# Optimization experiments

Hardware: AMD Instinct MI355X
Metric: run time of the kernel (lower is better)

Reference implementation:

```python
import jax, jax.numpy as jnp
import numpy as np
import math

N, E, IN, OUT, T, R = 50000, 500000, 128, 128, 8, 8
SQRT_DK = math.sqrt(OUT)


def setup_inputs() -> dict:
    key = jax.random.key(0)
    ks = jax.random.split(key, 12)
    return {
        "h": jax.random.normal(ks[0], (N, IN), jnp.float32),
        "adj": jax.random.randint(ks[1], (2, E), 0, N),
        "edge_type": jax.random.randint(ks[2], (E,), 0, R),
        "node_type": jax.random.randint(ks[3], (N,), 0, T),
        "src_type": jax.random.randint(ks[4], (E,), 0, T),
        "dst_type": jax.random.randint(ks[5], (E,), 0, T),
        # params (torch.rand -> uniform[0,1), torch.ones -> ones)
        "k_weights": jax.random.uniform(ks[6], (T, IN, OUT), jnp.float32),
        "q_weights": jax.random.uniform(ks[7], (T, IN, OUT), jnp.float32),
        "v_weights": jax.random.uniform(ks[8], (T, IN, OUT), jnp.float32),
        "a_weights": jax.random.uniform(ks[9], (T, OUT, OUT), jnp.float32),
        "relation_pri": jnp.ones((R, 1), jnp.float32),
        "relation_att": jax.random.uniform(ks[10], (R, OUT, OUT), jnp.float32),
        "relation_msg": jax.random.uniform(ks[11], (R, OUT, OUT), jnp.float32),
        "skip": jnp.ones((T,), jnp.float32),
    }


def _per_type(x, W, types):
    # x: [N,d], W: [T,d,f], types: [N] -> [N,f]
    # project by every type then select; avoids materializing a [N,d,f] gather
    all_proj = jnp.einsum('nd,tdf->tnf', x, W)  # [T,N,f]
    return all_proj[types, jnp.arange(x.shape[0])]


def _segment_softmax(scores, seg, num_segments):
    m = jax.ops.segment_max(scores, seg, num_segments=num_segments)
    m = jnp.where(jnp.isfinite(m), m, 0.0)  # empty segments
    ex = jnp.exp(scores - m[seg])
    denom = jax.ops.segment_sum(ex, seg, num_segments=num_segments)
    return ex / denom[seg]


def reference(h, adj, edge_type, node_type, src_type, dst_type,
              k_weights, q_weights, v_weights, a_weights,
              relation_pri, relation_att, relation_msg, skip):
    n = h.shape[0]
    src, dst = adj[0], adj[1]
    # per-node-type K/Q/V projections
    k = _per_type(h, k_weights, node_type)  # [N,OUT]
    q = _per_type(h, q_weights, node_type)
    v = _per_type(h, v_weights, node_type)
    # per-relation projections computed on nodes, then gathered per edge
    # (equivalent to k_j @ relation_att[edge_type] without an [E,D,D] gather)
    kA = jnp.einsum('nd,rdf->rnf', k, relation_att)[edge_type, src]  # [E,OUT]
    vM = jnp.einsum('nd,rdf->rnf', v, relation_msg)[edge_type, src]  # [E,OUT]
    q_i = q[dst]                                                     # [E,OUT]
    score = jnp.sum(kA * q_i, axis=-1) * relation_pri[edge_type, 0] / SQRT_DK  # [E]
    seg = dst * R + edge_type  # segment softmax keyed by (dst node, rel type)
    alpha = _segment_softmax(score, seg, n * R)  # [E]
    agg = jax.ops.segment_sum(vM * alpha[:, None], dst, num_segments=n)  # [N,OUT]
    # update: per-node-type output transform with sigmoid(skip) gate
    trans = _per_type(agg, a_weights, node_type)
    return trans * jax.nn.sigmoid(skip[node_type])[:, None]
```

## Files before the change

### kernel.cpp

```cpp
#include <hip/hip_runtime.h>
#include <math.h>


#define N_NODES 50000
#define N_EDGES 500000
#define DIM 128
#define TT 8
#define RR 8
#define RSQRT_DK 0.08838834764831845f

#define CHUNK_GRID 399
#define NODE_LIST_LEN (CHUNK_GRID * 128)
#define GRID_E ((N_EDGES + 255) / 256)
#define SCAN_BLOCKS ((N_NODES + 255) / 256)

#define NR3_CHUNKS 112
#define NR3_ROWS 448
#define NR3_ITERS 7

#define OFF_U 0
#define OFF_HF 0
#define OFF_VM 25600000
#define OFF_QF 48000000
#define OFF_KF 51200000
#define OFF_AGGF 54400000
#define OFF_VF 54400000
#define OFF_ATTF 57600000
#define OFF_MSGT 57700000
#define OFF_WVT 57800000
#define OFF_WAT 57900000
#define OFF_INT 58000000
#define IO_NLIST 0
#define IO_CNT_N 51072
#define IO_CUR_N 51080
#define IO_POFF_N 51088
#define IO_DCNT 51104
#define IO_DCUR 101104
#define IO_DOFF 151104
#define IO_DPR 201104
#define IO_BLKSUM 701104
#define IO_BLKOFF 701360

typedef _Float16 half8 __attribute__((ext_vector_type(8)));
typedef _Float16 half4 __attribute__((ext_vector_type(4)));
typedef float f32x4 __attribute__((ext_vector_type(4)));

__global__ void init_kernel(int* wsi) {
    int i = blockIdx.x * blockDim.x + threadIdx.x;
    if (i < NODE_LIST_LEN) wsi[IO_NLIST + i] = -1;
    if (i < 32) wsi[IO_CNT_N + i] = 0;
    if (i < 100000) wsi[IO_DCNT + i] = 0;
}

__global__ void convert_kernel(const float* __restrict__ att,
                               const float* __restrict__ msg,
                               const float* __restrict__ Wv,
                               const float* __restrict__ Wa,
                               _Float16* __restrict__ attF,
                               _Float16* __restrict__ msgT,
                               _Float16* __restrict__ WvT,
                               _Float16* __restrict__ WaT) {
    int i = blockIdx.x * 256 + threadIdx.x;
    if (i >= RR * DIM * DIM) return;
    int td = i >> 14, d = (i >> 7) & 127, f = i & 127;
    int tr = (td << 14) + (f << 7) + d;
    attF[i] = (_Float16)att[i];
    msgT[tr] = (_Float16)msg[i];
    WvT[tr] = (_Float16)Wv[i];
    WaT[tr] = (_Float16)Wa[i];
}

__global__ void hconv_kernel(const float* __restrict__ h,
                             _Float16* __restrict__ hF) {
    int i = blockIdx.x * 256 + threadIdx.x;
    if (i < N_NODES * DIM / 4) {
        float4 v = ((const float4*)h)[i];
        half4 o;
        o[0] = (_Float16)v.x; o[1] = (_Float16)v.y;
        o[2] = (_Float16)v.z; o[3] = (_Float16)v.w;
        *(half4*)(hF + (size_t)i * 4) = o;
    }
}

__global__ void hist_kernel(const int* __restrict__ ntype,
                            const int* __restrict__ adj, int* wsi) {
    __shared__ int cn[TT];
    int tid = threadIdx.x;
    if (tid < TT) cn[tid] = 0;
    __syncthreads();
    int i = blockIdx.x * blockDim.x + tid;
    if (i < N_NODES) atomicAdd(&cn[ntype[i]], 1);
    if (i < N_EDGES) atomicAdd(&wsi[IO_DCNT + adj[N_EDGES + i]], 1);
    __syncthreads();
    if (tid < TT && cn[tid] > 0) atomicAdd(&wsi[IO_CNT_N + tid], cn[tid]);
}

__global__ void offsets_kernel(int* wsi) {
    int off = 0;
    for (int t = 0; t < TT; ++t) {
        wsi[IO_POFF_N + t] = off;
        off += ((wsi[IO_CNT_N + t] + 127) >> 7) << 7;
    }
}

__global__ __launch_bounds__(256) void scanA_kernel(int* wsi) {
    __shared__ int tmp[256];
    int tid = threadIdx.x;
    int i = blockIdx.x * 256 + tid;
    int v = (i < N_NODES) ? wsi[IO_DCNT + i] : 0;
    tmp[tid] = v;
    __syncthreads();
    for (int off = 1; off < 256; off <<= 1) {
        int t = (tid >= off) ? tmp[tid - off] : 0;
        __syncthreads();
        tmp[tid] += t;
        __syncthreads();
    }
    if (i < N_NODES) wsi[IO_DOFF + i] = tmp[tid] - v;
    if (tid == 255) wsi[IO_BLKSUM + blockIdx.x] = tmp[255];
}

__global__ __launch_bounds__(256) void scanB_kernel(int* wsi) {
    __shared__ int tmp[256];
    int tid = threadIdx.x;
    int v = (tid < SCAN_BLOCKS) ? wsi[IO_BLKSUM + tid] : 0;
    tmp[tid] = v;
    __syncthreads();
    for (int off = 1; off < 256; off <<= 1) {
        int t = (tid >= off) ? tmp[tid - off] : 0;
        __syncthreads();
        tmp[tid] += t;
        __syncthreads();
    }
    wsi[IO_BLKOFF + tid] = tmp[tid] - v;
}

__global__ __launch_bounds__(256) void scanC_kernel(int* wsi) {
    int i = blockIdx.x * 256 + threadIdx.x;
    if (i < N_NODES) wsi[IO_DOFF + i] += wsi[IO_BLKOFF + blockIdx.x];
}

__global__ void scatter_kernel(const int* __restrict__ ntype,
                               const int* __restrict__ etype,
                               const int* __restrict__ adj, int* wsi) {
    __shared__ int cn[TT], bn[TT];
    int tid = threadIdx.x;
    if (tid < TT) cn[tid] = 0;
    __syncthreads();
    int i = blockIdx.x * blockDim.x + tid;
    int t = -1, rnk = 0;
    if (i < N_NODES) {
        t = ntype[i];
        rnk = atomicAdd(&cn[t], 1);
    }
    __syncthreads();
    if (tid < TT && cn[tid] > 0) bn[tid] = atomicAdd(&wsi[IO_CUR_N + tid], cn[tid]);
    __syncthreads();
    if (t >= 0)
        wsi[IO_NLIST + wsi[IO_POFF_N + t] + bn[t] + rnk] = i;
    if (i < N_EDGES) {
        int d = adj[N_EDGES + i];
        int pos = wsi[IO_DOFF + d] + atomicAdd(&wsi[IO_DCUR + d], 1);
        wsi[IO_DPR + pos] = (adj[i] << 3) | etype[i];
    }
}

__global__ __launch_bounds__(256, 4) void kq_f32_kernel(
    const float* __restrict__ h, const int* __restrict__ ntype,
    const float* __restrict__ Wk, const float* __restrict__ Wq,
    const int* __restrict__ nlist, _Float16* __restrict__ kout,
    _Float16* __restrict__ qout) {
    __shared__ float hl[64][DIM + 4];
    __shared__ int nid[64];
    int tid = threadIdx.x;
    int base = blockIdx.x * 64;
    if (tid < 64) nid[tid] = nlist[base + tid];
    __syncthreads();
    if (nid[0] < 0) return;
    int t = ntype[nid[0]];

    for (int r2 = 0; r2 < 64; r2 += 2) {
        int row = r2 + (tid >> 7);
        int col = tid & 127;
        int n = nid[row];
        if (n < 0) n = 0;
        hl[row][col] = h[(size_t)n * DIM + col];
    }
    __syncthreads();
    int te = tid >> 5, tc = tid & 31;

    int w = blockIdx.y;
    const float* W = (w == 0 ? Wk : Wq) + (size_t)t * DIM * DIM;
    const float4* W4 = (const float4*)W;
    _Float16* O = (w == 0 ? kout : qout);
    float acc[8][4] = {};
    float4 cur0 = W4[0 * 32 + tc];
    float4 cur1 = W4[1 * 32 + tc];
    float4 cur2 = W4[2 * 32 + tc];
    float4 cur3 = W4[3 * 32 + tc];
    for (int i = 0; i < DIM; i += 4) {
        int ip = (i + 4 < DIM) ? (i + 4) : 0;
        float4 nxt0 = W4[(ip + 0) * 32 + tc];
        float4 nxt1 = W4[(ip + 1) * 32 + tc];
        float4 nxt2 = W4[(ip + 2) * 32 + tc];
        float4 nxt3 = W4[(ip + 3) * 32 + tc];
#pragma unroll
        for (int j = 0; j < 8; ++j) {
            float4 hv = *(const float4*)&hl[te * 8 + j][i];
            acc[j][0] += hv.x * cur0.x;
            acc[j][1] += hv.x * cur0.y;
            acc[j][2] += hv.x * cur0.z;
            acc[j][3] += hv.x * cur0.w;
            acc[j][0] += hv.y * cur1.x;
            acc[j][1] += hv.y * cur1.y;
            acc[j][2] += hv.y * cur1.z;
            acc[j][3] += hv.y * cur1.w;
            acc[j][0] += hv.z * cur2.x;
            acc[j][1] += hv.z * cur2.y;
            acc[j][2] += hv.z * cur2.z;
            acc[j][3] += hv.z * cur2.w;
            acc[j][0] += hv.w * cur3.x;
            acc[j][1] += hv.w * cur3.y;
            acc[j][2] += hv.w * cur3.z;
            acc[j][3] += hv.w * cur3.w;
        }
        cur0 = nxt0;
        cur1 = nxt1;
        cur2 = nxt2;
        cur3 = nxt3;
    }
#pragma unroll
    for (int j = 0; j < 8; ++j) {
        int n = nid[te * 8 + j];
        if (n >= 0) {
            half4 o;
            o[0] = (_Float16)acc[j][0];
            o[1] = (_Float16)acc[j][1];
            o[2] = (_Float16)acc[j][2];
            o[3] = (_Float16)acc[j][3];
            *(half4*)(O + (size_t)n * DIM + tc * 4) = o;
        }
    }
}

__global__ __launch_bounds__(256) void vproj_kernel(
    const _Float16* __restrict__ hF, const int* __restrict__ ntype,
    const _Float16* __restrict__ WvT, const int* __restrict__ nlist,
    _Float16* __restrict__ vout) {
    __shared__ int nid[128];
    int tid = threadIdx.x;
    if (tid < 128) nid[tid] = nlist[blockIdx.x * 128 + tid];
    __syncthreads();
    if (nid[0] < 0) return;
    int t = ntype[nid[0]];
    int wv = tid >> 6, lane = tid & 63, l16 = lane & 15, quad = lane >> 4;
    int r0 = wv * 32;
    int nA[2];
#pragma unroll
    for (int m = 0; m < 2; ++m) nA[m] = nid[r0 + m * 16 + l16];
    const _Float16* B = WvT + (t << 14);
    f32x4 acc[2][8];
#pragma unroll
    for (int m = 0; m < 2; ++m)
#pragma unroll
        for (int c = 0; c < 8; ++c) acc[m][c] = (f32x4){0.f, 0.f, 0.f, 0.f};
    for (int kk = 0; kk < 4; ++kk) {
        int kb = kk * 32 + quad * 8;
        half8 a[2];
#pragma unroll
        for (int m = 0; m < 2; ++m)
            a[m] = (nA[m] >= 0)
                       ? *(const half8*)(hF + (size_t)nA[m] * DIM + kb)
                       : (half8){0, 0, 0, 0, 0, 0, 0, 0};
#pragma unroll
        for (int c = 0; c < 8; ++c) {
            half8 b = *(const half8*)(B + (c * 16 + l16) * DIM + kb);
#pragma unroll
            for (int m = 0; m < 2; ++m)
                acc[m][c] = __builtin_amdgcn_mfma_f32_16x16x32_f16(
                    a[m], b, acc[m][c], 0, 0, 0);
        }
    }
#pragma unroll
    for (int m = 0; m < 2; ++m)
#pragma unroll
        for (int c = 0; c < 8; ++c)
#pragma unroll
            for (int rg = 0; rg < 4; ++rg) {
                int node = nid[r0 + m * 16 + quad * 4 + rg];
                if (node >= 0)
                    vout[(size_t)node * DIM + c * 16 + l16] =
                        (_Float16)acc[m][c][rg];
            }
}

__global__ __launch_bounds__(256, 2) void nr_gemm3_kernel(
    const _Float16* __restrict__ A, const _Float16* __restrict__ B8,
    _Float16* __restrict__ Out, const float* __restrict__ pri, int isU) {
    __shared__ _Float16 stage[4][16][136];
    int bid = blockIdx.x;
    int rel = bid / NR3_CHUNKS;
    int chunk = bid - rel * NR3_CHUNKS;
    float scale = isU ? pri[rel] * RSQRT_DK : 1.0f;
    const _Float16* Bb = B8 + (rel << 14);
    int tid = threadIdx.x;
    int wv = tid >> 6, lane = tid & 63;
    int l16 = lane & 15, quad = lane >> 4;

    half8 bfrag[8][4];
#pragma unroll
    for (int c = 0; c < 8; ++c)
#pragma unroll
        for (int kk = 0; kk < 4; ++kk)
            bfrag[c][kk] =
                *(const half8*)(Bb + (c * 16 + l16) * DIM + kk * 32 + quad * 8);

    _Float16* Orel = Out + (size_t)rel * N_NODES * DIM;
    int base = chunk * NR3_ROWS + wv * 16;

    half8 aNow[4], aNext[4];
    {
        int nodeA = base + l16;
#pragma unroll
        for (int kk = 0; kk < 4; ++kk)
            aNow[kk] = (nodeA < N_NODES)
                           ? *(const half8*)(A + (size_t)nodeA * DIM +
                                             kk * 32 + quad * 8)
                           : (half8){0, 0, 0, 0, 0, 0, 0, 0};
    }

    for (int it = 0; it < NR3_ITERS; ++it) {
        int row0 = base + it * 64;
        if (it + 1 < NR3_ITERS) {
            int nodeA = row0 + 64 + l16;
#pragma unroll
            for (int kk = 0; kk < 4; ++kk)
                aNext[kk] = (nodeA < N_NODES)
                                ? *(const half8*)(A + (size_t)nodeA * DIM +
                                                  kk * 32 + quad * 8)
                                : (half8){0, 0, 0, 0, 0, 0, 0, 0};
        }
        f32x4 acc[8];
#pragma unroll
        for (int c = 0; c < 8; ++c) acc[c] = (f32x4){0.f, 0.f, 0.f, 0.f};
#pragma unroll
        for (int kk = 0; kk < 4; ++kk)
#pragma unroll
            for (int c = 0; c < 8; ++c)
                acc[c] = __builtin_amdgcn_mfma_f32_16x16x32_f16(
                    bfrag[c][kk], aNow[kk], acc[c], 0, 0, 0);
#pragma unroll
        for (int c = 0; c < 8; ++c) {
            half4 o;
#pragma unroll
            for (int rg = 0; rg < 4; ++rg)
                o[rg] = (_Float16)(acc[c][rg] * scale);
            *(half4*)&stage[wv][l16][c * 16 + quad * 4] = o;
        }
        _Float16* Op = Orel + (size_t)row0 * DIM;
#pragma unroll
        for (int s = 0; s < 4; ++s) {
            int row = s * 4 + quad;
            if (row0 + row < N_NODES) {
                half8 v = *(const half8*)&stage[wv][row][l16 * 8];
                *(half8*)(Op + (size_t)row * DIM + l16 * 8) = v;
            }
        }
#pragma unroll
        for (int kk = 0; kk < 4; ++kk) aNow[kk] = aNext[kk];
    }
}

__global__ __launch_bounds__(256) void attend_kernel(
    const _Float16* __restrict__ kF, const _Float16* __restrict__ UF,
    const _Float16* __restrict__ VMF, const int* __restrict__ dpr,
    const int* __restrict__ doff, const int* __restrict__ dcnt,
    _Float16* __restrict__ aggF) {
    int wv = threadIdx.x >> 6, lane = threadIdx.x & 63;
    int dst = blockIdx.x * 4 + wv;
    if (dst >= N_NODES) return;
    int l16 = lane & 15, g = lane >> 4, l8 = lane & 7;
    int beg = doff[dst], cnt = dcnt[dst];

    float m_own = -3e38f, sum_own = 0.f;
    float s0 = 0.f, s1 = 0.f, s2 = 0.f;
    int p0 = 0, p1 = 0, p2 = 0;

    for (int j0 = 0; j0 < cnt; j0 += 4) {
        int j = j0 + g;
        bool valid = j < cnt;
        int pr = valid ? dpr[beg + j] : 0;
        int src = pr >> 3, rel = pr & 7;
        half8 kv = *(const half8*)(kF + (size_t)src * DIM + l16 * 8);
        half8 uv = *(const half8*)(UF + ((size_t)rel * N_NODES + dst) * DIM +
                                   l16 * 8);
        float s = 0.f;
#pragma unroll
        for (int i = 0; i < 8; ++i) s += (float)kv[i] * (float)uv[i];
        s += __shfl_xor(s, 1, 16);
        s += __shfl_xor(s, 2, 16);
        s += __shfl_xor(s, 4, 16);
        s += __shfl_xor(s, 8, 16);
        if (!valid) s = -3e38f;
        int slot = j0 >> 6;
        int idx = (j0 >> 2) & 15;
        if (l16 == idx) {
            if (slot == 0) { s0 = s; p0 = pr; }
            else if (slot == 1) { s1 = s; p1 = pr; }
            else if (slot == 2) { s2 = s; p2 = pr; }
        }
        if (valid && l8 == rel && s > m_own) m_own = s;
    }
    m_own = fmaxf(m_own, __shfl_xor(m_own, 16, 64));
    m_own = fmaxf(m_own, __shfl_xor(m_own, 32, 64));

    for (int j0 = 0; j0 < cnt; j0 += 4) {
        int j = j0 + g;
        bool valid = j < cnt;
        int slot = j0 >> 6;
        int idx = (j0 >> 2) & 15;
        float s;
        int pr;
        if (slot < 3) {
            float sv = (slot == 0) ? s0 : (slot == 1) ? s1 : s2;
            int pv = (slot == 0) ? p0 : (slot == 1) ? p1 : p2;
            s = __shfl(sv, idx, 16);
            pr = __shfl(pv, idx, 16);
        } else {
            pr = valid ? dpr[beg + j] : 0;
            int src = pr >> 3, rel = pr & 7;
            half8 kv = *(const half8*)(kF + (size_t)src * DIM + l16 * 8);
            half8 uv = *(const half8*)(UF +
                                       ((size_t)rel * N_NODES + dst) * DIM +
                                       l16 * 8);
            s = 0.f;
#pragma unroll
            for (int i = 0; i < 8; ++i) s += (float)kv[i] * (float)uv[i];
            s += __shfl_xor(s, 1, 16);
            s += __shfl_xor(s, 2, 16);
            s += __shfl_xor(s, 4, 16);
            s += __shfl_xor(s, 8, 16);
        }
        int rel = pr & 7;
        float mr = __shfl(m_own, rel, 8);
        float ex = valid ? __expf(s - mr) : 0.f;
        if (l16 == idx) {
            if (slot == 0) s0 = ex;
            else if (slot == 1) s1 = ex;
            else if (slot == 2) s2 = ex;
        }
        if (l8 == rel) sum_own += ex;
    }
    sum_own += __shfl_xor(sum_own, 16, 64);
    sum_own += __shfl_xor(sum_own, 32, 64);
    float inv_own = (sum_own > 0.f) ? 1.f / sum_own : 0.f;

    float acc[8] = {0.f, 0.f, 0.f, 0.f, 0.f, 0.f, 0.f, 0.f};
    for (int j0 = 0; j0 < cnt; j0 += 4) {
        int j = j0 + g;
        bool valid = j < cnt;
        int slot = j0 >> 6;
        int idx = (j0 >> 2) & 15;
        float ex;
        int pr;
        if (slot < 3) {
            float sv = (slot == 0) ? s0 : (slot == 1) ? s1 : s2;
            int pv = (slot == 0) ? p0 : (slot == 1) ? p1 : p2;
            ex = __shfl(sv, idx, 16);
            pr = __shfl(pv, idx, 16);
        } else {
            pr = valid ? dpr[beg + j] : 0;
            int src = pr >> 3, rel = pr & 7;
            half8 kv = *(const half8*)(kF + (size_t)src * DIM + l16 * 8);
            half8 uv = *(const half8*)(UF +
                                       ((size_t)rel * N_NODES + dst) * DIM +
                                       l16 * 8);
            float s = 0.f;
#pragma unroll
            for (int i = 0; i < 8; ++i) s += (float)kv[i] * (float)uv[i];
            s += __shfl_xor(s, 1, 16);
            s += __shfl_xor(s, 2, 16);
            s += __shfl_xor(s, 4, 16);
            s += __shfl_xor(s, 8, 16);
            float mr = __shfl(m_own, (pr & 7), 8);
            ex = valid ? __expf(s - mr) : 0.f;
        }
        int rel = pr & 7, src = pr >> 3;
        float alpha = ex * __shfl(inv_own, rel, 8);
        half8 v = *(const half8*)(VMF + ((size_t)rel * N_NODES + src) * DIM +
                                  l16 * 8);
#pragma unroll
        for (int i = 0; i < 8; ++i) acc[i] += alpha * (float)v[i];
    }
#pragma unroll
    for (int i = 0; i < 8; ++i) {
        acc[i] += __shfl_xor(acc[i], 16, 64);
        acc[i] += __shfl_xor(acc[i], 32, 64);
    }
    if (g == 0) {
        half8 o;
#pragma unroll
        for (int i = 0; i < 8; ++i) o[i] = (_Float16)acc[i];
        *(half8*)(aggF + (size_t)dst * DIM + l16 * 8) = o;
    }
}

__global__ __launch_bounds__(256) void out_kernel(
    const _Float16* __restrict__ aggF, const int* __restrict__ ntype,
    const _Float16* __restrict__ WaT, const float* __restrict__ skip,
    const int* __restrict__ nlist, float* __restrict__ out) {
    __shared__ int nid[128];
    int tid = threadIdx.x;
    if (tid < 128) nid[tid] = nlist[blockIdx.x * 128 + tid];
    __syncthreads();
    if (nid[0] < 0) return;
    int t = ntype[nid[0]];
    float sig = 1.f / (1.f + __expf(-skip[t]));
    int wv = tid >> 6, lane = tid & 63, l16 = lane & 15, quad = lane >> 4;
    int r0 = wv * 32;
    int nA[2];
#pragma unroll
    for (int m = 0; m < 2; ++m) nA[m] = nid[r0 + m * 16 + l16];
    const _Float16* B = WaT + (t << 14);
    f32x4 acc[2][8];
#pragma unroll
    for (int m = 0; m < 2; ++m)
#pragma unroll
        for (int c = 0; c < 8; ++c) acc[m][c] = (f32x4){0.f, 0.f, 0.f, 0.f};
    for (int kk = 0; kk < 4; ++kk) {
        int kb = kk * 32 + quad * 8;
        half8 a[2];
#pragma unroll
        for (int m = 0; m < 2; ++m)
            a[m] = (nA[m] >= 0)
                       ? *(const half8*)(aggF + (size_t)nA[m] * DIM + kb)
                       : (half8){0, 0, 0, 0, 0, 0, 0, 0};
#pragma unroll
        for (int c = 0; c < 8; ++c) {
            half8 b = *(const half8*)(B + (c * 16 + l16) * DIM + kb);
#pragma unroll
            for (int m = 0; m < 2; ++m)
                acc[m][c] = __builtin_amdgcn_mfma_f32_16x16x32_f16(
                    a[m], b, acc[m][c], 0, 0, 0);
        }
    }
#pragma unroll
    for (int m = 0; m < 2; ++m)
#pragma unroll
        for (int c = 0; c < 8; ++c)
#pragma unroll
            for (int rg = 0; rg < 4; ++rg) {
                int node = nid[r0 + m * 16 + quad * 4 + rg];
                if (node >= 0)
                    out[(size_t)node * DIM + c * 16 + l16] =
                        acc[m][c][rg] * sig;
            }
}

extern "C" void kernel_launch(void* const* d_in, const int* in_sizes, int n_in,
                              void* d_out, int out_size, void* d_ws,
                              size_t ws_size, hipStream_t stream) {
    const float* h = (const float*)d_in[0];
    const int* adj = (const int*)d_in[1];
    const int* etype = (const int*)d_in[2];
    const int* ntype = (const int*)d_in[3];
    const float* Wk = (const float*)d_in[6];
    const float* Wq = (const float*)d_in[7];
    const float* Wv = (const float*)d_in[8];
    const float* Wa = (const float*)d_in[9];
    const float* pri = (const float*)d_in[10];
    const float* att = (const float*)d_in[11];
    const float* msg = (const float*)d_in[12];
    const float* skip = (const float*)d_in[13];
    float* out = (float*)d_out;

    int* wsi = (int*)d_ws + OFF_INT;
    _Float16* wsh = (_Float16*)d_ws;
    _Float16* UF = wsh + (size_t)OFF_U * 2;
    _Float16* hF = wsh + (size_t)OFF_HF * 2;
    _Float16* VMF = wsh + (size_t)OFF_VM * 2;
    _Float16* qF = wsh + (size_t)OFF_QF * 2;
    _Float16* kF = wsh + (size_t)OFF_KF * 2;
    _Float16* aggF = wsh + (size_t)OFF_AGGF * 2;
    _Float16* vF = wsh + (size_t)OFF_VF * 2;
    _Float16* attF = wsh + (size_t)OFF_ATTF * 2;
    _Float16* msgT = wsh + (size_t)OFF_MSGT * 2;
    _Float16* WvT = wsh + (size_t)OFF_WVT * 2;
    _Float16* WaT = wsh + (size_t)OFF_WAT * 2;

    init_kernel<<<(100000 + 255) / 256, 256, 0, stream>>>(wsi);
    convert_kernel<<<(RR * DIM * DIM + 255) / 256, 256, 0, stream>>>(
        att, msg, Wv, Wa, attF, msgT, WvT, WaT);
    hconv_kernel<<<(N_NODES * DIM / 4 + 255) / 256, 256, 0, stream>>>(h, hF);
    hist_kernel<<<GRID_E, 256, 0, stream>>>(ntype, adj, wsi);
    offsets_kernel<<<1, 1, 0, stream>>>(wsi);
    scanA_kernel<<<SCAN_BLOCKS, 256, 0, stream>>>(wsi);
    scanB_kernel<<<1, 256, 0, stream>>>(wsi);
    scanC_kernel<<<SCAN_BLOCKS, 256, 0, stream>>>(wsi);
    scatter_kernel<<<GRID_E, 256, 0, stream>>>(ntype, etype, adj, wsi);
    {
        dim3 g(CHUNK_GRID * 2, 2);
        kq_f32_kernel<<<g, 256, 0, stream>>>(h, ntype, Wk, Wq,
                                             wsi + IO_NLIST, kF, qF);
    }
    vproj_kernel<<<CHUNK_GRID, 256, 0, stream>>>(hF, ntype, WvT,
                                                 wsi + IO_NLIST, vF);
    nr_gemm3_kernel<<<RR * NR3_CHUNKS, 256, 0, stream>>>(qF, attF, UF, pri, 1);
    nr_gemm3_kernel<<<RR * NR3_CHUNKS, 256, 0, stream>>>(vF, msgT, VMF, pri, 0);
    attend_kernel<<<(N_NODES + 3) / 4, 256, 0, stream>>>(
        kF, UF, VMF, wsi + IO_DPR, wsi + IO_DOFF, wsi + IO_DCNT, aggF);
    out_kernel<<<CHUNK_GRID, 256, 0, stream>>>(aggF, ntype, WaT, skip,
                                               wsi + IO_NLIST, out);
}
```

Baseline: 383.9 us.

## Fuse softmax max and sum passes with online softmax and stage U in LDS

The attend kernel now computes the per-relation max and exp-sum in a single online-softmax pass, merging partial states across lane groups with rescaling. This removes the separate pass that only computed exp sums. It also stages the destination node's eight U rows in shared memory once per wave instead of reading them from global memory for every edge. The cost is extra exp calls per edge in the first pass and more LDS use per block, which could lower occupancy.

```diff
diff --git a/kernel.cpp b/kernel.cpp
--- a/kernel.cpp
+++ b/kernel.cpp
@@ -376,11 +376,20 @@
     const _Float16* __restrict__ VMF, const int* __restrict__ dpr,
     const int* __restrict__ doff, const int* __restrict__ dcnt,
     _Float16* __restrict__ aggF) {
+    __shared__ _Float16 uls[4][8][136];
     int wv = threadIdx.x >> 6, lane = threadIdx.x & 63;
     int dst = blockIdx.x * 4 + wv;
     if (dst >= N_NODES) return;
     int l16 = lane & 15, g = lane >> 4, l8 = lane & 7;
     int beg = doff[dst], cnt = dcnt[dst];
+
+    {
+        int rr = lane >> 3;
+        int c0 = (lane & 7) * 16;
+        const _Float16* Ur = UF + ((size_t)rr * N_NODES + dst) * DIM + c0;
+        *(half8*)&uls[wv][rr][c0] = *(const half8*)Ur;
+        *(half8*)&uls[wv][rr][c0 + 8] = *(const half8*)(Ur + 8);
+    }
 
     float m_own = -3e38f, sum_own = 0.f;
     float s0 = 0.f, s1 = 0.f, s2 = 0.f;
@@ -392,11 +401,13 @@
         int pr = valid ? dpr[beg + j] : 0;
         int src = pr >> 3, rel = pr & 7;
         half8 kv = *(const half8*)(kF + (size_t)src * DIM + l16 * 8);
-        half8 uv = *(const half8*)(UF + ((size_t)rel * N_NODES + dst) * DIM +
-                                   l16 * 8);
-        float s = 0.f;
-#pragma unroll
-        for (int i = 0; i < 8; ++i) s += (float)kv[i] * (float)uv[i];
+        half8 uv = *(const half8*)&uls[wv][rel][l16 * 8];
+        float sa = 0.f, sb = 0.f;
+#pragma unroll
+        for (int i = 0; i < 4; ++i) sa += (float)kv[i] * (float)uv[i];
+#pragma unroll
+        for (int i = 4; i < 8; ++i) sb += (float)kv[i] * (float)uv[i];
+        float s = sa + sb;
         s += __shfl_xor(s, 1, 16);
         s += __shfl_xor(s, 2, 16);
         s += __shfl_xor(s, 4, 16);
@@ -409,11 +420,29 @@
             else if (slot == 1) { s1 = s; p1 = pr; }
             else if (slot == 2) { s2 = s; p2 = pr; }
         }
-        if (valid && l8 == rel && s > m_own) m_own = s;
-    }
-    m_own = fmaxf(m_own, __shfl_xor(m_own, 16, 64));
-    m_own = fmaxf(m_own, __shfl_xor(m_own, 32, 64));
-
+        if (valid && l8 == rel) {
+            if (s > m_own) {
+                sum_own *= __expf(m_own - s);
+                m_own = s;
+            }
+            sum_own += __expf(s - m_own);
+        }
+    }
+    {
+        float m2 = __shfl_xor(m_own, 16, 64);
+        float t2 = __shfl_xor(sum_own, 16, 64);
+        float mn = fmaxf(m_own, m2);
+        sum_own = sum_own * __expf(m_own - mn) + t2 * __expf(m2 - mn);
+        m_own = mn;
+        m2 = __shfl_xor(m_own, 32, 64);
+        t2 = __shfl_xor(sum_own, 32, 64);
+        mn = fmaxf(m_own, m2);
+        sum_own = sum_own * __expf(m_own - mn) + t2 * __expf(m2 - mn);
+        m_own = mn;
+    }
+    float inv_own = (sum_own > 0.f) ? 1.f / sum_own : 0.f;
+
+    float acc[8] = {0.f, 0.f, 0.f, 0.f, 0.f, 0.f, 0.f, 0.f};
     for (int j0 = 0; j0 < cnt; j0 += 4) {
         int j = j0 + g;
         bool valid = j < cnt;
@@ -430,63 +459,22 @@
             pr = valid ? dpr[beg + j] : 0;
             int src = pr >> 3, rel = pr & 7;
             half8 kv = *(const half8*)(kF + (size_t)src * DIM + l16 * 8);
-            half8 uv = *(const half8*)(UF +
-                                       ((size_t)rel * N_NODES + dst) * DIM +
-                                       l16 * 8);
-            s = 0.f;
-#pragma unroll
-            for (int i = 0; i < 8; ++i) s += (float)kv[i] * (float)uv[i];
+            half8 uv = *(const half8*)&uls[wv][rel][l16 * 8];
+            float sa = 0.f, sb = 0.f;
+#pragma unroll
+            for (int i = 0; i < 4; ++i) sa += (float)kv[i] * (float)uv[i];
+#pragma unroll
+            for (int i = 4; i < 8; ++i) sb += (float)kv[i] * (float)uv[i];
+            s = sa + sb;
             s += __shfl_xor(s, 1, 16);
             s += __shfl_xor(s, 2, 16);
             s += __shfl_xor(s, 4, 16);
             s += __shfl_xor(s, 8, 16);
         }
-        int rel = pr & 7;
+        int rel = pr & 7, src = pr >> 3;
         float mr = __shfl(m_own, rel, 8);
-        float ex = valid ? __expf(s - mr) : 0.f;
-        if (l16 == idx) {
-            if (slot == 0) s0 = ex;
-            else if (slot == 1) s1 = ex;
-            else if (slot == 2) s2 = ex;
-        }
-        if (l8 == rel) sum_own += ex;
-    }
-    sum_own += __shfl_xor(sum_own, 16, 64);
-    sum_own += __shfl_xor(sum_own, 32, 64);
-    float inv_own = (sum_own > 0.f) ? 1.f / sum_own : 0.f;
-
-    float acc[8] = {0.f, 0.f, 0.f, 0.f, 0.f, 0.f, 0.f, 0.f};
-    for (int j0 = 0; j0 < cnt; j0 += 4) {
-        int j = j0 + g;
-        bool valid = j < cnt;
-        int slot = j0 >> 6;
-        int idx = (j0 >> 2) & 15;
-        float ex;
-        int pr;
-        if (slot < 3) {
-            float sv = (slot == 0) ? s0 : (slot == 1) ? s1 : s2;
-            int pv = (slot == 0) ? p0 : (slot == 1) ? p1 : p2;
-            ex = __shfl(sv, idx, 16);
-            pr = __shfl(pv, idx, 16);
-        } else {
-            pr = valid ? dpr[beg + j] : 0;
-            int src = pr >> 3, rel = pr & 7;
-            half8 kv = *(const half8*)(kF + (size_t)src * DIM + l16 * 8);
-            half8 uv = *(const half8*)(UF +
-                                       ((size_t)rel * N_NODES + dst) * DIM +
-                                       l16 * 8);
-            float s = 0.f;
-#pragma unroll
-            for (int i = 0; i < 8; ++i) s += (float)kv[i] * (float)uv[i];
-            s += __shfl_xor(s, 1, 16);
-            s += __shfl_xor(s, 2, 16);
-            s += __shfl_xor(s, 4, 16);
-            s += __shfl_xor(s, 8, 16);
-            float mr = __shfl(m_own, (pr & 7), 8);
-            ex = valid ? __expf(s - mr) : 0.f;
-        }
-        int rel = pr & 7, src = pr >> 3;
-        float alpha = ex * __shfl(inv_own, rel, 8);
+        float iv = __shfl(inv_own, rel, 8);
+        float alpha = valid ? __expf(s - mr) * iv : 0.f;
         half8 v = *(const half8*)(VMF + ((size_t)rel * N_NODES + src) * DIM +
                                   l16 * 8);
 #pragma unroll
```

Result: no change. 384.0 us (+0.0%).
